# Optimization experiments

Hardware: AMD Instinct MI355X
Metric: run time of the kernel (lower is better)

The kernel has to match this reference:

```python
import jax, jax.numpy as jnp
import numpy as np

LN_EPS = 1e-5


def setup_inputs() -> dict:
    key = jax.random.key(0)
    ks = jax.random.split(key, 6)
    B, S, Dv, Dk, A = 32, 2048, 1024, 1024, 1024
    meta_state = jax.random.normal(ks[0], (B, S, Dv), dtype=jnp.float32)
    hidden_previous = jax.random.normal(ks[1], (B, Dk), dtype=jnp.float32)
    # torch nn.Linear weights are [out_features, in_features]
    WK = jax.random.normal(ks[2], (A, Dv), dtype=jnp.float32) * (1.0 / np.sqrt(Dv))
    WQ = jax.random.normal(ks[3], (A, Dk), dtype=jnp.float32) * (1.0 / np.sqrt(Dk))
    WV = jax.random.normal(ks[4], (Dv, Dv), dtype=jnp.float32) * (1.0 / np.sqrt(Dv))
    WO = jax.random.normal(ks[5], (Dv, Dv), dtype=jnp.float32) * (1.0 / np.sqrt(Dv))
    ln_w = jnp.ones((Dv,), dtype=jnp.float32)
    ln_b = jnp.zeros((Dv,), dtype=jnp.float32)
    return {"meta_state": meta_state, "hidden_previous": hidden_previous,
            "WK": WK, "WQ": WQ, "WV": WV, "WO": WO, "ln_w": ln_w, "ln_b": ln_b}


def reference(meta_state, hidden_previous, WK, WQ, WV, WO, ln_w, ln_b):
    A = WK.shape[0]
    scale = 1.0 / jnp.sqrt(jnp.asarray(A, dtype=meta_state.dtype))
    # projections
    K = jnp.einsum('bsd,ad->bsa', meta_state, WK)          # [B,S,A]
    q = jnp.einsum('bd,ad->ba', hidden_previous, WQ)       # [B,A]
    V = jnp.einsum('bsd,ed->bse', meta_state, WV)          # [B,S,Dv]
    # single-query attention over sequence dim
    logits = jnp.einsum('bsa,ba->bs', K, q) * scale        # [B,S]
    weight = jax.nn.softmax(logits, axis=1)                # softmax over S (dim=1)
    attention = jnp.einsum('bse,bs->be', V, weight)        # [B,Dv]
    # output layer: Linear(no bias) -> Tanh -> LayerNorm (dropout = identity in eval)
    h = jnp.tanh(attention @ WO.T)
    mu = jnp.mean(h, axis=-1, keepdims=True)
    var = jnp.mean(jnp.square(h - mu), axis=-1, keepdims=True)
    out = (h - mu) / jnp.sqrt(var + LN_EPS) * ln_w + ln_b  # [B,Dv]
    return out, weight[..., None]                          # weight shape [B,S,1] as in torch
```

## Files before the change

kernel.cpp:

```cpp
#include <hip/hip_runtime.h>
#include <math.h>

#define B 32
#define S 2048
#define D 1024
#define CPB 32
#define CHROWS (S / CPB)
#define WROWS (CHROWS / 4)
#define ACH 16
#define SCALE (1.0f / 32.0f)
#define LN_EPS 1e-5f

__device__ __forceinline__ float wave_sum(float v) {
#pragma unroll
  for (int off = 32; off > 0; off >>= 1) v += __shfl_xor(v, off, 64);
  return v;
}

__global__ __launch_bounds__(128) void gemm_xw(const float* __restrict__ X,
                                               const float* __restrict__ W,
                                               float* __restrict__ Y,
                                               const int do_tanh) {
  const int tid = blockIdx.x * 128 + threadIdx.x;
  const int b = tid & (B - 1);
  const int r = tid >> 5;
  const float4* x4 = (const float4*)(X + (size_t)b * D);
  const float4* w4 = (const float4*)(W + (size_t)r * D);
  float acc = 0.f;
#pragma unroll 8
  for (int k = 0; k < D / 4; ++k) {
    float4 a = x4[k];
    float4 w = w4[k];
    acc += a.x * w.x + a.y * w.y + a.z * w.z + a.w * w.w;
  }
  if (do_tanh) acc = tanhf(acc);
  Y[(size_t)b * D + r] = acc;
}

__global__ __launch_bounds__(256) void kq_partial(const float* __restrict__ q,
                                                  const float* __restrict__ WK,
                                                  float* __restrict__ kqp) {
  const int t = threadIdx.x, ac = blockIdx.x, bg = blockIdx.y;
  const int d0 = t * 4;
  float accx[8] = {}, accy[8] = {}, accz[8] = {}, accw[8] = {};
  const int a0 = ac * (1024 / ACH);
  for (int a = a0; a < a0 + (1024 / ACH); ++a) {
    float4 wk = *(const float4*)(WK + (size_t)a * D + d0);
#pragma unroll
    for (int j = 0; j < 8; ++j) {
      float qv = q[(size_t)(bg * 8 + j) * D + a];
      accx[j] += qv * wk.x;
      accy[j] += qv * wk.y;
      accz[j] += qv * wk.z;
      accw[j] += qv * wk.w;
    }
  }
#pragma unroll
  for (int j = 0; j < 8; ++j) {
    float4 o;
    o.x = accx[j]; o.y = accy[j]; o.z = accz[j]; o.w = accw[j];
    *(float4*)(kqp + ((size_t)ac * B + bg * 8 + j) * D + d0) = o;
  }
}

__global__ __launch_bounds__(256) void kq_reduce(const float* __restrict__ kqp,
                                                 float* __restrict__ kq) {
  const int i4 = (blockIdx.x * 256 + threadIdx.x) * 4;
  float sx = 0.f, sy = 0.f, sz = 0.f, sw = 0.f;
  for (int c = 0; c < ACH; ++c) {
    float4 v = *(const float4*)(kqp + (size_t)c * (B * D) + i4);
    sx += v.x; sy += v.y; sz += v.z; sw += v.w;
  }
  float4 o;
  o.x = sx; o.y = sy; o.z = sz; o.w = sw;
  *(float4*)(kq + i4) = o;
}

__global__ __launch_bounds__(256) void attn_main(
    const float* __restrict__ meta, const float* __restrict__ kq,
    float* __restrict__ logits_out, float* __restrict__ cm,
    float* __restrict__ cl, float* __restrict__ cacc) {
  const int c = blockIdx.x, b = blockIdx.y;
  const int t = threadIdx.x, w = t >> 6, lane = t & 63;
  const int row0 = c * CHROWS + w * WROWS;
  const float* base = meta + ((size_t)b * S + row0) * D + lane * 4;

  float4 kqf[4];
#pragma unroll
  for (int j = 0; j < 4; ++j)
    kqf[j] = *(const float4*)(kq + (size_t)b * D + j * 256 + lane * 4);

  float4 acc[4] = {};
  float m = -INFINITY, l = 0.f;

  float4 v[4], vn[4];
#pragma unroll
  for (int j = 0; j < 4; ++j) v[j] = *(const float4*)(base + j * 256);

  for (int s = 0; s < WROWS; ++s) {
    const float* nb = base + (size_t)(s + 1 < WROWS ? s + 1 : s) * D;
#pragma unroll
    for (int j = 0; j < 4; ++j) vn[j] = *(const float4*)(nb + j * 256);

    float p = 0.f;
#pragma unroll
    for (int j = 0; j < 4; ++j)
      p += v[j].x * kqf[j].x + v[j].y * kqf[j].y + v[j].z * kqf[j].z +
           v[j].w * kqf[j].w;
    p = wave_sum(p);
    const float logit = p * SCALE;
    if (lane == 0) logits_out[(size_t)b * S + row0 + s] = logit;

    if (logit > m) {
      const float f = expf(m - logit);
#pragma unroll
      for (int j = 0; j < 4; ++j) {
        acc[j].x *= f; acc[j].y *= f; acc[j].z *= f; acc[j].w *= f;
      }
      l *= f;
      m = logit;
    }
    const float p2 = expf(logit - m);
#pragma unroll
    for (int j = 0; j < 4; ++j) {
      acc[j].x += p2 * v[j].x; acc[j].y += p2 * v[j].y;
      acc[j].z += p2 * v[j].z; acc[j].w += p2 * v[j].w;
    }
    l += p2;
#pragma unroll
    for (int j = 0; j < 4; ++j) v[j] = vn[j];
  }

  __shared__ float lds_acc[4][D];
  __shared__ float lds_m[4], lds_l[4];
  if (lane == 0) { lds_m[w] = m; lds_l[w] = l; }
#pragma unroll
  for (int j = 0; j < 4; ++j)
    *(float4*)(&lds_acc[w][j * 256 + lane * 4]) = acc[j];
  __syncthreads();

  const float M = fmaxf(fmaxf(lds_m[0], lds_m[1]), fmaxf(lds_m[2], lds_m[3]));
  float fac[4], L = 0.f;
#pragma unroll
  for (int w2 = 0; w2 < 4; ++w2) {
    fac[w2] = expf(lds_m[w2] - M);
    L += lds_l[w2] * fac[w2];
  }
  float4 sv = {};
#pragma unroll
  for (int w2 = 0; w2 < 4; ++w2) {
    float4 a = *(const float4*)(&lds_acc[w2][t * 4]);
    sv.x += fac[w2] * a.x; sv.y += fac[w2] * a.y;
    sv.z += fac[w2] * a.z; sv.w += fac[w2] * a.w;
  }
  const int pc = b * CPB + c;
  *(float4*)(cacc + (size_t)pc * D + t * 4) = sv;
  if (t == 0) { cm[pc] = M; cl[pc] = L; }
}

__global__ __launch_bounds__(256) void combine(const float* __restrict__ cm,
                                               const float* __restrict__ cl,
                                               const float* __restrict__ cacc,
                                               float* __restrict__ wio,
                                               float* __restrict__ wm) {
  const int b = blockIdx.x, t = threadIdx.x;
  float M = -INFINITY;
  for (int c2 = 0; c2 < CPB; ++c2) M = fmaxf(M, cm[b * CPB + c2]);
  float L = 0.f;
  for (int c2 = 0; c2 < CPB; ++c2) L += cl[b * CPB + c2] * expf(cm[b * CPB + c2] - M);
  const float invL = 1.0f / L;

  float sx = 0.f, sy = 0.f, sz = 0.f, sw = 0.f;
  for (int c2 = 0; c2 < CPB; ++c2) {
    const float f = expf(cm[b * CPB + c2] - M);
    float4 a = *(const float4*)(cacc + ((size_t)b * CPB + c2) * D + 4 * t);
    sx += f * a.x; sy += f * a.y; sz += f * a.z; sw += f * a.w;
  }
  float4 o;
  o.x = sx * invL; o.y = sy * invL; o.z = sz * invL; o.w = sw * invL;
  *(float4*)(wm + (size_t)b * D + 4 * t) = o;

  for (int s = t; s < S; s += 256) {
    const float lg = wio[(size_t)b * S + s];
    wio[(size_t)b * S + s] = expf(lg - M) * invL;
  }
}

__global__ __launch_bounds__(256) void ln_kernel(const float* __restrict__ h,
                                                 const float* __restrict__ lnw,
                                                 const float* __restrict__ lnb,
                                                 float* __restrict__ out) {
  const int b = blockIdx.x, t = threadIdx.x, wid = t >> 6, lane = t & 63;
  __shared__ float r1[4], r2[4];
  float4 v = *(const float4*)(h + (size_t)b * D + 4 * t);
  float s1 = v.x + v.y + v.z + v.w;
  float s2 = v.x * v.x + v.y * v.y + v.z * v.z + v.w * v.w;
  s1 = wave_sum(s1);
  s2 = wave_sum(s2);
  if (lane == 0) { r1[wid] = s1; r2[wid] = s2; }
  __syncthreads();
  const float mean = (r1[0] + r1[1] + r1[2] + r1[3]) * (1.0f / D);
  const float ms = (r2[0] + r2[1] + r2[2] + r2[3]) * (1.0f / D);
  const float var = ms - mean * mean;
  const float rstd = rsqrtf(var + LN_EPS);
  float4 w = *(const float4*)(lnw + 4 * t);
  float4 bb = *(const float4*)(lnb + 4 * t);
  float4 o;
  o.x = (v.x - mean) * rstd * w.x + bb.x;
  o.y = (v.y - mean) * rstd * w.y + bb.y;
  o.z = (v.z - mean) * rstd * w.z + bb.z;
  o.w = (v.w - mean) * rstd * w.w + bb.w;
  *(float4*)(out + (size_t)b * D + 4 * t) = o;
}

extern "C" void kernel_launch(void* const* d_in, const int* in_sizes, int n_in,
                              void* d_out, int out_size, void* d_ws,
                              size_t ws_size, hipStream_t stream) {
  (void)in_sizes; (void)n_in; (void)out_size; (void)ws_size;
  const float* meta   = (const float*)d_in[0];
  const float* hidden = (const float*)d_in[1];
  const float* WK = (const float*)d_in[2];
  const float* WQ = (const float*)d_in[3];
  const float* WV = (const float*)d_in[4];
  const float* WO = (const float*)d_in[5];
  const float* lnw = (const float*)d_in[6];
  const float* lnb = (const float*)d_in[7];

  float* out  = (float*)d_out;
  float* wout = out + B * D;

  float* ws   = (float*)d_ws;
  float* q    = ws;
  float* kqp  = q + B * D;
  float* kq   = kqp + (size_t)ACH * B * D;
  float* cm   = kq + B * D;
  float* cl   = cm + B * CPB;
  float* cacc = cl + B * CPB;
  float* wm   = cacc + (size_t)B * CPB * D;
  float* att  = wm + B * D;
  float* h    = att + B * D;

  gemm_xw<<<dim3((B * D) / 128), 128, 0, stream>>>(hidden, WQ, q, 0);
  kq_partial<<<dim3(ACH, 4), 256, 0, stream>>>(q, WK, kqp);
  kq_reduce<<<dim3((B * D) / 1024), 256, 0, stream>>>(kqp, kq);
  attn_main<<<dim3(CPB, B), 256, 0, stream>>>(meta, kq, wout, cm, cl, cacc);
  combine<<<dim3(B), 256, 0, stream>>>(cm, cl, cacc, wout, wm);
  gemm_xw<<<dim3((B * D) / 128), 128, 0, stream>>>(wm, WV, att, 0);
  gemm_xw<<<dim3((B * D) / 128), 128, 0, stream>>>(att, WO, h, 1);
  ln_kernel<<<dim3(B), 256, 0, stream>>>(h, lnw, lnb, out);
}
```

Measured before the change: 511.2 us.

## Raise parallelism across attention chunks, GEMV split-K, reduce and combine kernels

```diff
diff --git a/kernel.cpp b/kernel.cpp
--- a/kernel.cpp
+++ b/kernel.cpp
@@ -4,7 +4,7 @@
 #define B 32
 #define S 2048
 #define D 1024
-#define CPB 32
+#define CPB 64
 #define CHROWS (S / CPB)
 #define WROWS (CHROWS / 4)
 #define ACH 16
@@ -17,24 +17,32 @@
   return v;
 }
 
-__global__ __launch_bounds__(128) void gemm_xw(const float* __restrict__ X,
+__global__ __launch_bounds__(256) void gemm_xw(const float* __restrict__ X,
                                                const float* __restrict__ W,
                                                float* __restrict__ Y,
                                                const int do_tanh) {
-  const int tid = blockIdx.x * 128 + threadIdx.x;
-  const int b = tid & (B - 1);
-  const int r = tid >> 5;
-  const float4* x4 = (const float4*)(X + (size_t)b * D);
-  const float4* w4 = (const float4*)(W + (size_t)r * D);
+  const int t = threadIdx.x;
+  const int b = t & 31;
+  const int rr = (t >> 5) & 3;
+  const int kh = t >> 7;
+  const int r = blockIdx.x * 4 + rr;
+  const float4* x4 = (const float4*)(X + (size_t)b * D + kh * (D / 2));
+  const float4* w4 = (const float4*)(W + (size_t)r * D + kh * (D / 2));
   float acc = 0.f;
 #pragma unroll 8
-  for (int k = 0; k < D / 4; ++k) {
+  for (int k = 0; k < D / 8; ++k) {
     float4 a = x4[k];
     float4 w = w4[k];
     acc += a.x * w.x + a.y * w.y + a.z * w.z + a.w * w.w;
   }
-  if (do_tanh) acc = tanhf(acc);
-  Y[(size_t)b * D + r] = acc;
+  __shared__ float part[256];
+  part[t] = acc;
+  __syncthreads();
+  if (kh == 0) {
+    float v = part[t] + part[t + 128];
+    if (do_tanh) v = tanhf(v);
+    Y[(size_t)b * D + r] = v;
+  }
 }
 
 __global__ __launch_bounds__(256) void kq_partial(const float* __restrict__ q,
@@ -63,9 +71,9 @@
   }
 }
 
-__global__ __launch_bounds__(256) void kq_reduce(const float* __restrict__ kqp,
-                                                 float* __restrict__ kq) {
-  const int i4 = (blockIdx.x * 256 + threadIdx.x) * 4;
+__global__ __launch_bounds__(64) void kq_reduce(const float* __restrict__ kqp,
+                                                float* __restrict__ kq) {
+  const int i4 = (blockIdx.x * 64 + threadIdx.x) * 4;
   float sx = 0.f, sy = 0.f, sz = 0.f, sw = 0.f;
   for (int c = 0; c < ACH; ++c) {
     float4 v = *(const float4*)(kqp + (size_t)c * (B * D) + i4);
@@ -158,29 +166,28 @@
   if (t == 0) { cm[pc] = M; cl[pc] = L; }
 }
 
-__global__ __launch_bounds__(256) void combine(const float* __restrict__ cm,
+__global__ __launch_bounds__(128) void combine(const float* __restrict__ cm,
                                                const float* __restrict__ cl,
                                                const float* __restrict__ cacc,
                                                float* __restrict__ wio,
                                                float* __restrict__ wm) {
-  const int b = blockIdx.x, t = threadIdx.x;
+  const int b = blockIdx.x, dt = blockIdx.y, t = threadIdx.x;
   float M = -INFINITY;
   for (int c2 = 0; c2 < CPB; ++c2) M = fmaxf(M, cm[b * CPB + c2]);
+  __shared__ float fac[CPB];
+  if (t < CPB) fac[t] = expf(cm[b * CPB + t] - M);
+  __syncthreads();
   float L = 0.f;
-  for (int c2 = 0; c2 < CPB; ++c2) L += cl[b * CPB + c2] * expf(cm[b * CPB + c2] - M);
+  for (int c2 = 0; c2 < CPB; ++c2) L += cl[b * CPB + c2] * fac[c2];
   const float invL = 1.0f / L;
 
-  float sx = 0.f, sy = 0.f, sz = 0.f, sw = 0.f;
-  for (int c2 = 0; c2 < CPB; ++c2) {
-    const float f = expf(cm[b * CPB + c2] - M);
-    float4 a = *(const float4*)(cacc + ((size_t)b * CPB + c2) * D + 4 * t);
-    sx += f * a.x; sy += f * a.y; sz += f * a.z; sw += f * a.w;
-  }
-  float4 o;
-  o.x = sx * invL; o.y = sy * invL; o.z = sz * invL; o.w = sw * invL;
-  *(float4*)(wm + (size_t)b * D + 4 * t) = o;
-
-  for (int s = t; s < S; s += 256) {
+  const int d = dt * 128 + t;
+  float sv = 0.f;
+  for (int c2 = 0; c2 < CPB; ++c2)
+    sv += fac[c2] * cacc[((size_t)b * CPB + c2) * D + d];
+  wm[(size_t)b * D + d] = sv * invL;
+
+  for (int s = dt * 256 + t; s < dt * 256 + 256; s += 128) {
     const float lg = wio[(size_t)b * S + s];
     wio[(size_t)b * S + s] = expf(lg - M) * invL;
   }
@@ -240,12 +247,12 @@
   float* att  = wm + B * D;
   float* h    = att + B * D;
 
-  gemm_xw<<<dim3((B * D) / 128), 128, 0, stream>>>(hidden, WQ, q, 0);
+  gemm_xw<<<dim3(D / 4), 256, 0, stream>>>(hidden, WQ, q, 0);
   kq_partial<<<dim3(ACH, 4), 256, 0, stream>>>(q, WK, kqp);
-  kq_reduce<<<dim3((B * D) / 1024), 256, 0, stream>>>(kqp, kq);
+  kq_reduce<<<dim3((B * D) / 256), 64, 0, stream>>>(kqp, kq);
   attn_main<<<dim3(CPB, B), 256, 0, stream>>>(meta, kq, wout, cm, cl, cacc);
-  combine<<<dim3(B), 256, 0, stream>>>(cm, cl, cacc, wout, wm);
-  gemm_xw<<<dim3((B * D) / 128), 128, 0, stream>>>(wm, WV, att, 0);
-  gemm_xw<<<dim3((B * D) / 128), 128, 0, stream>>>(att, WO, h, 1);
+  combine<<<dim3(B, 8), 128, 0, stream>>>(cm, cl, cacc, wout, wm);
+  gemm_xw<<<dim3(D / 4), 256, 0, stream>>>(wm, WV, att, 0);
+  gemm_xw<<<dim3(D / 4), 256, 0, stream>>>(att, WO, h, 1);
   ln_kernel<<<dim3(B), 256, 0, stream>>>(h, lnw, lnb, out);
 }
```

Result: faster. 475.6 us (-7.0%).
